# Kernel optimization log

Measured on AMD Instinct MI355X. Metric: run time of the kernel, lower is better.

The kernel has to match this reference:

```python
import jax, jax.numpy as jnp
import numpy as np

N_NODES = 128   # num_nodes
BATCH = 4096
HIDDEN = 32     # fixed by the module's Linear(N+1, 32)


def setup_inputs() -> dict:
    key = jax.random.key(0)
    ks = jax.random.split(key, 8)
    N, B, H = N_NODES, BATCH, HIDDEN
    x = jax.random.normal(ks[0], (B, N), dtype=jnp.float32)
    # adjacency masks: A[b, :, j] = parent indicator of node j in sample b
    A = (jax.random.uniform(ks[1], (B, N, N)) < 0.3).astype(jnp.float32)
    # per-sample topological permutation
    order = jax.vmap(lambda k: jax.random.permutation(k, N))(
        jax.random.split(ks[2], B)).astype(jnp.int32)
    # intervention target per sample, -1 = no intervention
    do_idxs = jax.random.randint(ks[3], (B,), -1, N, dtype=jnp.int32)
    # externalized intervention noise (torch.normal in the original forward)
    u = jax.random.normal(ks[4], (B,), dtype=jnp.float32)
    # stacked per-node MLP params: Linear(N+1, 32) -> LeakyReLU -> Linear(32, 1)
    W1 = jax.random.normal(ks[5], (N, N + 1, H), dtype=jnp.float32) / np.sqrt(N + 1)
    b1 = jnp.zeros((N, H), dtype=jnp.float32)
    W2 = jax.random.normal(ks[6], (N, H, 1), dtype=jnp.float32) / np.sqrt(H)
    b2 = jnp.zeros((N, 1), dtype=jnp.float32)
    return dict(x=x, A=A, u=u, W1=W1, b1=b1, W2=W2, b2=b2,
                order=order, do_idxs=do_idxs)


def reference(x, A, u, W1, b1, W2, b2, order, do_idxs):
    B, N = x.shape
    bidx = jnp.arange(B)
    # set intervened entries: outputs[b, do_idxs[b]] = u[b] where do_idxs != -1
    outputs0 = jnp.where(do_idxs[:, None] == jnp.arange(N)[None, :],
                         u[:, None], jnp.zeros_like(x))

    def step(outputs, node):           # node: [B] current node per sample
        mask = A[bidx, :, node]        # [B, N] parent mask of this node
        ins = jnp.concatenate([mask * outputs,
                               x[bidx, node][:, None]], axis=1)  # [B, N+1]
        # per-node MLP gathered by node id (grouped tiny GEMMs)
        h = jax.nn.leaky_relu(jnp.einsum('bd,bdh->bh', ins, W1[node]) + b1[node])
        out = (jnp.einsum('bh,bho->bo', h, W2[node]) + b2[node])[:, 0]  # [B]
        # intervened samples keep their value u (they are skipped in the original)
        new_val = jnp.where(do_idxs == node, outputs[bidx, node], out)
        return outputs.at[bidx, node].set(new_val), None

    outputs, _ = jax.lax.scan(step, outputs0, order.T)  # sequential topo order
    return outputs
```

## Files before the change

### kernel.cpp

```cpp
#include <hip/hip_runtime.h>
#include <stdint.h>

#define NN 128
#define BB 4096
#define HH 32

typedef float f4 __attribute__((ext_vector_type(4)));

__global__ __launch_bounds__(256) void pack_bits(const float* __restrict__ A,
                                                 ulonglong2* __restrict__ bitsT) {
    const int tid = blockIdx.x * 256 + threadIdx.x;
    const int b  = tid >> 7;
    const int q  = (tid >> 5) & 3;
    const int ng = (tid & 31) << 2;
    const float* Ab = A + (size_t)b * (NN * NN) + (size_t)(q * 32) * NN + ng;
    unsigned int w[4] = {0u, 0u, 0u, 0u};
#pragma unroll 8
    for (int d = 0; d < 32; ++d) {
        f4 v = __builtin_nontemporal_load((const f4*)(Ab + (size_t)d * NN));
        const unsigned int bit = 1u << d;
        if (v[0] != 0.f) w[0] |= bit;
        if (v[1] != 0.f) w[1] |= bit;
        if (v[2] != 0.f) w[2] |= bit;
        if (v[3] != 0.f) w[3] |= bit;
    }
    unsigned int* o = (unsigned int*)(bitsT + (size_t)b * NN + ng);
#pragma unroll
    for (int i = 0; i < 4; ++i) o[i * 4 + q] = w[i];
}

__device__ __forceinline__ int mbcnt64(unsigned long long m) {
    return __builtin_amdgcn_mbcnt_hi((unsigned int)(m >> 32),
           __builtin_amdgcn_mbcnt_lo((unsigned int)m, 0));
}
__device__ __forceinline__ unsigned long long rfl64(unsigned long long v) {
    unsigned int lo = __builtin_amdgcn_readfirstlane((unsigned int)v);
    unsigned int hi = __builtin_amdgcn_readfirstlane((unsigned int)(v >> 32));
    return ((unsigned long long)hi << 32) | lo;
}

struct Pipe {
    int node;
    int cnt;
    unsigned long long bw0, bw1;
    ulonglong2 vb;
    float w2v, b1v, xv, b2v, w1xv, wfr;
};

#define STEP(T, ECUR, ENXT, SC, SN, BCUR, BNXT)                              \
  {                                                                          \
    const int nodeT = SC.node;                                               \
    const char* WnB = (const char*)(W1 + (size_t)nodeT * ((NN + 1) * HH));   \
                                                                      \
    float wv[16];                                                            \
    _Pragma("unroll")                                                        \
    for (int q = 0; q < 8; ++q) {                                            \
        wv[2*q]   = *(const float*)(WnB + (__float_as_int(ECUR[q][1]) + j4));\
        wv[2*q+1] = *(const float*)(WnB + (__float_as_int(ECUR[q][3]) + j4));\
    }                                                                        \
                                                                      \
    if ((T) > 0) {                                                           \
        if (dob != pend_node && lane == (pend_node & 63)) {                  \
            if (pend_node < 64) out0 = pend_val; else out1 = pend_val;       \
        }                                                                    \
        if (pend_node < 64) nz0 |= 1ull << pend_node;                        \
        else                nz1 |= 1ull << (pend_node - 64);                 \
    }                                                                        \
                                                                      \
    const unsigned long long bw0n = rfl64(SN.vb.x);                          \
    const unsigned long long bw1n = rfl64(SN.vb.y);                          \
    const unsigned long long m0 = nz0 & bw0n;                                \
    const unsigned long long m1 = nz1 & bw1n;                                \
    const int c0n  = __popcll(m0);                                           \
    const int cntn = c0n + __popcll(m1);                                     \
    SN.bw0 = bw0n; SN.bw1 = bw1n; SN.cnt = cntn;                             \
                                                                      \
    {                                                                        \
        const int p0 = mbcnt64(m0);                                          \
        if (m0 & lanebit)                                                    \
            entb[BNXT][p0 & 1][p0 >> 1] = make_float2(out0, fidx0);          \
        const int p1 = c0n + mbcnt64(m1);                                    \
        if (m1 & lanebit)                                                    \
            entb[BNXT][p1 & 1][p1 >> 1] = make_float2(out1, fidx1);          \
        const int top = (cntn > 32) ? 48 : 32;                               \
        const int pp = cntn + lane;                                          \
        if (pp < top)                                                        \
            entb[BNXT][pp & 1][pp >> 1] = make_float2(0.f, __int_as_float(0));\
    }                                                                        \
                                                                      \
    {                                                                        \
        const f4* eb = (const f4*)&entb[BNXT][half][0];                      \
        _Pragma("unroll")                                                    \
        for (int q = 0; q < 8; ++q) ENXT[q] = eb[q];                         \
    }                                                                        \
                                                                      \
    const int node2 = ((T) + 2 < NN)                                         \
        ? __builtin_amdgcn_readfirstlane(ord[(T) + 2]) : 0;                  \
    SC.node = node2;                                                         \
    SC.vb   = bb[node2];                                                     \
    {                                                                        \
        const float* Wn_nxt = W1 + (size_t)SN.node * ((NN + 1) * HH);        \
        SN.w2v  = W2[SN.node * HH + j];                                      \
        SN.b1v  = b1[SN.node * HH + j];                                      \
        SN.xv   = x[b * NN + SN.node];                                       \
        SN.b2v  = b2[SN.node];                                               \
        SN.w1xv = Wn_nxt[NN * HH + j];                                       \
        SN.wfr  = Wn_nxt[(nodeT << 5) + j];                                  \
    }                                                                        \
                                                                      \
    float a0 = 0.f, a1 = 0.f, a2 = 0.f, a3 = 0.f;                            \
    _Pragma("unroll")                                                        \
    for (int q = 0; q < 8; q += 2) {                                         \
        a0 += ECUR[q][0]     * wv[2*q];                                      \
        a1 += ECUR[q][2]     * wv[2*q+1];                                    \
        a2 += ECUR[q+1][0]   * wv[2*q+2];                                    \
        a3 += ECUR[q+1][2]   * wv[2*q+3];                                    \
    }                                                                        \
                 \
    if (SC_cnt_snap > 32) {                                                  \
        f4 e3[4];                                                            \
        const f4* eb3 = (const f4*)&entb[BCUR][half][16];                    \
        _Pragma("unroll")                                                    \
        for (int q = 0; q < 4; ++q) e3[q] = eb3[q];                          \
        float w3[8];                                                         \
        _Pragma("unroll")                                                    \
        for (int q = 0; q < 4; ++q) {                                        \
            w3[2*q]   = *(const float*)(WnB + (__float_as_int(e3[q][1]) + j4));\
            w3[2*q+1] = *(const float*)(WnB + (__float_as_int(e3[q][3]) + j4));\
        }                                                                    \
        _Pragma("unroll")                                                    \
        for (int q = 0; q < 4; ++q) {                                        \
            a0 += e3[q][0] * w3[2*q];                                        \
            a1 += e3[q][2] * w3[2*q+1];                                      \
        }                                                                    \
             \
        if (SC_cnt_snap > 48) {                                              \
            for (int i = 24; 2 * i + half < SC_cnt_snap; ++i) {              \
                float2 e = entb[BCUR][half][i];                              \
                a2 += e.x * *(const float*)(WnB + (__float_as_int(e.y) + j4));\
            }                                                                \
        }                                                                    \
    }                                                                        \
    float acc = (a0 + a1) + (a2 + a3);                                       \
                                                                      \
    float accT = acc + __shfl_xor(acc, 32);                                  \
    const bool fc = ((T) > 0) && (dob != pend_node) &&                       \
        ((((pend_node < 64) ? (SC.bw0 >> pend_node)                          \
                            : (SC.bw1 >> (pend_node - 64)))) & 1ull);        \
    accT += (fc ? pend_val : 0.f) * SC.wfr;                                  \
    accT += SC.xv * SC.w1xv;                                                 \
    accT += SC.b1v;                                                          \
    const float hv = (accT > 0.f) ? accT : 0.01f * accT;                     \
    float pr = hv * SC.w2v;                                                  \
    pr += __int_as_float(__builtin_amdgcn_update_dpp(                        \
             0, __float_as_int(pr), 0xB1, 0xF, 0xF, true));                  \
    pr += __int_as_float(__builtin_amdgcn_update_dpp(                        \
             0, __float_as_int(pr), 0x4E, 0xF, 0xF, true));                  \
    pr += __int_as_float(__builtin_amdgcn_update_dpp(                        \
             0, __float_as_int(pr), 0x141, 0xF, 0xF, true));                 \
    pr += __int_as_float(__builtin_amdgcn_update_dpp(                        \
             0, __float_as_int(pr), 0x140, 0xF, 0xF, true));                 \
    pr += __shfl_xor(pr, 16);                                                \
    const float outv = pr + SC.b2v;                                          \
    pend_node = nodeT; pend_val = outv;                                      \
  }

__global__ __launch_bounds__(64, 4) void cond_mlp(
    const float* __restrict__ x, const float* __restrict__ u,
    const float* __restrict__ W1, const float* __restrict__ b1,
    const float* __restrict__ W2, const float* __restrict__ b2,
    const int* __restrict__ order, const int* __restrict__ do_idxs,
    const ulonglong2* __restrict__ bitsT, float* __restrict__ out)
{
    const int b = blockIdx.x;
    const int lane = threadIdx.x;
    const int j = lane & 31;
    const int j4 = j << 2;
    const int half = lane >> 5;

    __shared__ __align__(16) float2 entb[2][2][68];

    const float ub = u[b];
    const int dob = __builtin_amdgcn_readfirstlane(do_idxs[b]);
    float out0 = (dob == lane) ? ub : 0.f;
    float out1 = (dob == lane + 64) ? ub : 0.f;

    unsigned long long nz0 = (dob >= 0 && dob < 64) ? (1ull << dob) : 0ull;
    unsigned long long nz1 = (dob >= 64) ? (1ull << (dob - 64)) : 0ull;

    const int* ord = order + b * NN;
    const ulonglong2* bb = bitsT + (size_t)b * NN;

    const unsigned long long lanebit = 1ull << lane;
    const float fidx0 = __int_as_float(lane << 7);
    const float fidx1 = __int_as_float((lane + 64) << 7);

    Pipe SA, SB;
    SA.node = __builtin_amdgcn_readfirstlane(ord[0]);
    SB.node = __builtin_amdgcn_readfirstlane(ord[1]);
    SB.vb = bb[SB.node];
    SA.vb = bb[SA.node];

    SA.bw0 = rfl64(SA.vb.x);
    SA.bw1 = rfl64(SA.vb.y);
    f4 eA[8], eB[8];
    {
        const unsigned long long m0 = nz0 & SA.bw0;
        const unsigned long long m1 = nz1 & SA.bw1;
        const int c0 = __popcll(m0);
        SA.cnt = c0 + __popcll(m1);
        const int p0 = mbcnt64(m0);
        if (m0 & lanebit) entb[0][p0 & 1][p0 >> 1] = make_float2(out0, fidx0);
        const int p1 = c0 + mbcnt64(m1);
        if (m1 & lanebit) entb[0][p1 & 1][p1 >> 1] = make_float2(out1, fidx1);
        const int top = (SA.cnt > 32) ? 48 : 32;
        const int pp = SA.cnt + lane;
        if (pp < top) entb[0][pp & 1][pp >> 1] = make_float2(0.f, __int_as_float(0));
        const f4* eb = (const f4*)&entb[0][half][0];
#pragma unroll
        for (int q = 0; q < 8; ++q) eA[q] = eb[q];
    }
    {
        const float* Wn0 = W1 + (size_t)SA.node * ((NN + 1) * HH);
        SA.w2v  = W2[SA.node * HH + j];
        SA.b1v  = b1[SA.node * HH + j];
        SA.xv   = x[b * NN + SA.node];
        SA.b2v  = b2[SA.node];
        SA.w1xv = Wn0[NN * HH + j];
        SA.wfr  = 0.f;
    }

    int pend_node = 0;
    float pend_val = 0.f;

    for (int t = 0; t < NN; t += 2) {
        const int SC_cnt_snap0 = SA.cnt;
        { const int SC_cnt_snap = SC_cnt_snap0;
          STEP(t,     eA, eB, SA, SB, 0, 1) }
        const int SC_cnt_snap1 = SB.cnt;
        { const int SC_cnt_snap = SC_cnt_snap1;
          STEP(t + 1, eB, eA, SB, SA, 1, 0) }
    }

    if (dob != pend_node && lane == (pend_node & 63)) {
        if (pend_node < 64) out0 = pend_val; else out1 = pend_val;
    }

    out[b * NN + lane] = out0;
    out[b * NN + 64 + lane] = out1;
}

extern "C" void kernel_launch(void* const* d_in, const int* in_sizes, int n_in,
                              void* d_out, int out_size, void* d_ws, size_t ws_size,
                              hipStream_t stream) {
    const float* x   = (const float*)d_in[0];
    const float* A   = (const float*)d_in[1];
    const float* u   = (const float*)d_in[2];
    const float* W1  = (const float*)d_in[3];
    const float* b1  = (const float*)d_in[4];
    const float* W2  = (const float*)d_in[5];
    const float* b2  = (const float*)d_in[6];
    const int* order = (const int*)d_in[7];
    const int* dox   = (const int*)d_in[8];

    ulonglong2* bitsT = (ulonglong2*)d_ws;

    pack_bits<<<(BB * 128) / 256, 256, 0, stream>>>(A, bitsT);
    cond_mlp<<<BB, 64, 0, stream>>>(x, u, W1, b1, W2, b2, order, dox,
                                    bitsT, (float*)d_out);
}
```

Measured before the change: 516.6 us.

## Prefetch next step's gathered W1 weights one step ahead in register buffers

The 16 per-lane gathers of W1 rows for the first 32 parent entries are moved out of the current step. They are now issued for the next node right after its entry buffer is built, into double-buffered register arrays WA/WB. This aims to hide the global gather latency on the sequential topological chain behind the current step's dot product and reduction. It costs 16 extra live registers per lane, which may reduce occupancy. The cnt snapshot variables are replaced by direct reads of SC.cnt.

```diff
diff --git a/kernel.cpp b/kernel.cpp
--- a/kernel.cpp
+++ b/kernel.cpp
@@ -47,17 +47,9 @@
     float w2v, b1v, xv, b2v, w1xv, wfr;
 };
 
-#define STEP(T, ECUR, ENXT, SC, SN, BCUR, BNXT)                              \
+#define STEP(T, ECUR, ENXT, WCUR, WNXT, SC, SN, BCUR, BNXT)                  \
   {                                                                          \
     const int nodeT = SC.node;                                               \
-    const char* WnB = (const char*)(W1 + (size_t)nodeT * ((NN + 1) * HH));   \
-                                                                      \
-    float wv[16];                                                            \
-    _Pragma("unroll")                                                        \
-    for (int q = 0; q < 8; ++q) {                                            \
-        wv[2*q]   = *(const float*)(WnB + (__float_as_int(ECUR[q][1]) + j4));\
-        wv[2*q+1] = *(const float*)(WnB + (__float_as_int(ECUR[q][3]) + j4));\
-    }                                                                        \
                                                                       \
     if ((T) > 0) {                                                           \
         if (dob != pend_node && lane == (pend_node & 63)) {                  \
@@ -107,17 +99,29 @@
         SN.w1xv = Wn_nxt[NN * HH + j];                                       \
         SN.wfr  = Wn_nxt[(nodeT << 5) + j];                                  \
     }                                                                        \
-                                                                      \
+            \
+    {                                                                        \
+        const char* WnBn = (const char*)(W1 + (size_t)SN.node * ((NN+1)*HH));\
+        _Pragma("unroll")                                                    \
+        for (int q = 0; q < 8; ++q) {                                        \
+            WNXT[2*q]   = *(const float*)(WnBn +                             \
+                              (__float_as_int(ENXT[q][1]) + j4));            \
+            WNXT[2*q+1] = *(const float*)(WnBn +                             \
+                              (__float_as_int(ENXT[q][3]) + j4));            \
+        }                                                                    \
+    }                                                                        \
+                                           \
     float a0 = 0.f, a1 = 0.f, a2 = 0.f, a3 = 0.f;                            \
     _Pragma("unroll")                                                        \
     for (int q = 0; q < 8; q += 2) {                                         \
-        a0 += ECUR[q][0]     * wv[2*q];                                      \
-        a1 += ECUR[q][2]     * wv[2*q+1];                                    \
-        a2 += ECUR[q+1][0]   * wv[2*q+2];                                    \
-        a3 += ECUR[q+1][2]   * wv[2*q+3];                                    \
-    }                                                                        \
-                 \
-    if (SC_cnt_snap > 32) {                                                  \
+        a0 += ECUR[q][0]     * WCUR[2*q];                                    \
+        a1 += ECUR[q][2]     * WCUR[2*q+1];                                  \
+        a2 += ECUR[q+1][0]   * WCUR[2*q+2];                                  \
+        a3 += ECUR[q+1][2]   * WCUR[2*q+3];                                  \
+    }                                                                        \
+           \
+    if (SC.cnt > 32) {                                                       \
+        const char* WnB = (const char*)(W1 + (size_t)nodeT * ((NN+1)*HH));   \
         f4 e3[4];                                                            \
         const f4* eb3 = (const f4*)&entb[BCUR][half][16];                    \
         _Pragma("unroll")                                                    \
@@ -133,9 +137,9 @@
             a0 += e3[q][0] * w3[2*q];                                        \
             a1 += e3[q][2] * w3[2*q+1];                                      \
         }                                                                    \
-             \
-        if (SC_cnt_snap > 48) {                                              \
-            for (int i = 24; 2 * i + half < SC_cnt_snap; ++i) {              \
+                         \
+        if (SC.cnt > 48) {                                                   \
+            for (int i = 24; 2 * i + half < SC.cnt; ++i) {                   \
                 float2 e = entb[BCUR][half][i];                              \
                 a2 += e.x * *(const float*)(WnB + (__float_as_int(e.y) + j4));\
             }                                                                \
@@ -199,11 +203,12 @@
     SA.node = __builtin_amdgcn_readfirstlane(ord[0]);
     SB.node = __builtin_amdgcn_readfirstlane(ord[1]);
     SB.vb = bb[SB.node];
-    SA.vb = bb[SA.node];
-
-    SA.bw0 = rfl64(SA.vb.x);
-    SA.bw1 = rfl64(SA.vb.y);
+    const ulonglong2 vb0 = bb[SA.node];
+
+    SA.bw0 = rfl64(vb0.x);
+    SA.bw1 = rfl64(vb0.y);
     f4 eA[8], eB[8];
+    float WA[16], WB[16];
     {
         const unsigned long long m0 = nz0 & SA.bw0;
         const unsigned long long m1 = nz1 & SA.bw1;
@@ -221,6 +226,12 @@
         for (int q = 0; q < 8; ++q) eA[q] = eb[q];
     }
     {
+        const char* WnB0 = (const char*)(W1 + (size_t)SA.node * ((NN+1)*HH));
+#pragma unroll
+        for (int q = 0; q < 8; ++q) {
+            WA[2*q]   = *(const float*)(WnB0 + (__float_as_int(eA[q][1]) + j4));
+            WA[2*q+1] = *(const float*)(WnB0 + (__float_as_int(eA[q][3]) + j4));
+        }
         const float* Wn0 = W1 + (size_t)SA.node * ((NN + 1) * HH);
         SA.w2v  = W2[SA.node * HH + j];
         SA.b1v  = b1[SA.node * HH + j];
@@ -234,12 +245,8 @@
     float pend_val = 0.f;
 
     for (int t = 0; t < NN; t += 2) {
-        const int SC_cnt_snap0 = SA.cnt;
-        { const int SC_cnt_snap = SC_cnt_snap0;
-          STEP(t,     eA, eB, SA, SB, 0, 1) }
-        const int SC_cnt_snap1 = SB.cnt;
-        { const int SC_cnt_snap = SC_cnt_snap1;
-          STEP(t + 1, eB, eA, SB, SA, 1, 0) }
+        STEP(t,     eA, eB, WA, WB, SA, SB, 0, 1)
+        STEP(t + 1, eB, eA, WB, WA, SB, SA, 1, 0)
     }
 
     if (dob != pend_node && lane == (pend_node & 63)) {
```

New measurement: 528.1 us. +2.2%, slower.
